# Performance work log

Hardware: AMD Instinct MI355X
Metric: run time of the kernel (lower is better)

The kernel has to match this reference:

```python
import jax, jax.numpy as jnp
import numpy as np


def setup_inputs() -> dict:
    key = jax.random.key(0)
    k1, k2, k3 = jax.random.split(key, 3)
    B, F, D = 8192, 4096, 1024
    x = jax.random.normal(k1, (B, D), dtype=jnp.float32)
    mu = jax.random.normal(k2, (F, D), dtype=jnp.float32)
    # keep scales strictly positive and well-conditioned
    scale_diag = jax.random.uniform(k3, (F, D), dtype=jnp.float32, minval=0.5, maxval=1.5)
    return {"x": x, "mu": mu, "scale_diag": scale_diag}


def reference(x, mu, scale_diag):
    # Unnormalized diag-Gaussian log prob for every (batch, feature) pair:
    #   out[b, f] = sum_d -0.5 * ((x[b,d] - mu[f,d]) / scale[f,d])^2
    # Expanded to GEMM form (quadratic expansion):
    #   -0.5 * ( x^2 @ inv2.T  -  2 * x @ (mu*inv2).T  +  sum_d mu^2*inv2 )
    inv2 = 1.0 / (scale_diag * scale_diag)            # [F, D]
    xx = jnp.matmul(x * x, inv2.T)                    # [B, F]
    xm = jnp.matmul(x, (mu * inv2).T)                 # [B, F]
    mm = jnp.sum(mu * mu * inv2, axis=-1)             # [F]
    return -0.5 * (xx - 2.0 * xm + mm[None, :])       # [B, F]
```

## Files before the change

### kernel.cpp

```cpp
#include <hip/hip_runtime.h>
#include <hip/hip_bf16.h>
#include <cstdint>

#define B_SZ 8192
#define F_SZ 4096
#define D_SZ 1024
#define K_SZ 2048

typedef __bf16 bf16x8 __attribute__((ext_vector_type(8)));
typedef float f32x4 __attribute__((ext_vector_type(4)));

__device__ __forceinline__ unsigned short f2bf(float f) {
    union { float f; unsigned u; } c; c.f = f;
    unsigned r = c.u + 0x7fff + ((c.u >> 16) & 1);
    return (unsigned short)(r >> 16);
}

__device__ __forceinline__ void async16(const void* g, void* l) {
    __builtin_amdgcn_global_load_lds(
        (__attribute__((address_space(1))) void*)g,
        (__attribute__((address_space(3))) void*)l, 16, 0, 0);
}

__global__ __launch_bounds__(256) void prep_a(const float* __restrict__ x,
                                              unsigned short* __restrict__ A) {
    int gid = blockIdx.x * 256 + threadIdx.x;
    int idx4 = gid * 4;
    int b = idx4 >> 10;
    int d = idx4 & 1023;
    float4 v = *(const float4*)(x + idx4);
    ushort4 xx, xs;
    xx.x = f2bf(v.x * v.x); xx.y = f2bf(v.y * v.y);
    xx.z = f2bf(v.z * v.z); xx.w = f2bf(v.w * v.w);
    xs.x = f2bf(v.x); xs.y = f2bf(v.y); xs.z = f2bf(v.z); xs.w = f2bf(v.w);
    size_t base = (size_t)b * K_SZ;
    *(ushort4*)(A + base + d) = xx;
    *(ushort4*)(A + base + 1024 + d) = xs;
}

__global__ __launch_bounds__(256) void prep_w(const float* __restrict__ mu,
                                              const float* __restrict__ sd,
                                              unsigned short* __restrict__ W,
                                              float* __restrict__ nmm) {
    int f = blockIdx.x;
    int d = threadIdx.x * 4;
    size_t off = (size_t)f * D_SZ + d;
    float4 m = *(const float4*)(mu + off);
    float4 s = *(const float4*)(sd + off);
    float i0 = 1.0f / (s.x * s.x), i1 = 1.0f / (s.y * s.y);
    float i2 = 1.0f / (s.z * s.z), i3 = 1.0f / (s.w * s.w);
    ushort4 wi, wm;
    wi.x = f2bf(i0); wi.y = f2bf(i1); wi.z = f2bf(i2); wi.w = f2bf(i3);
    wm.x = f2bf(-2.0f * m.x * i0); wm.y = f2bf(-2.0f * m.y * i1);
    wm.z = f2bf(-2.0f * m.z * i2); wm.w = f2bf(-2.0f * m.w * i3);
    size_t wb = (size_t)f * K_SZ + d;
    *(ushort4*)(W + wb) = wi;
    *(ushort4*)(W + wb + 1024) = wm;
    float mm = m.x * m.x * i0 + m.y * m.y * i1 + m.z * m.z * i2 + m.w * m.w * i3;
    #pragma unroll
    for (int o = 32; o > 0; o >>= 1) mm += __shfl_down(mm, o, 64);
    __shared__ float red[4];
    if ((threadIdx.x & 63) == 0) red[threadIdx.x >> 6] = mm;
    __syncthreads();
    if (threadIdx.x == 0) nmm[f] = -0.5f * (red[0] + red[1] + red[2] + red[3]);
}

__global__ __launch_bounds__(256) void gemm_bt(const unsigned short* __restrict__ A,
                                               const unsigned short* __restrict__ W,
                                               const float* __restrict__ nmm,
                                               float* __restrict__ out) {
    __shared__ __align__(16) unsigned short sA[128 * 32];
    __shared__ __align__(16) unsigned short sB[128 * 32];

    const int tid  = threadIdx.x;
    const int wave = tid >> 6;
    const int lane = tid & 63;
    const int wm = (wave >> 1) * 64;
    const int wn = (wave & 1) * 64;
    const int tileM = blockIdx.y * 128;
    const int tileN = blockIdx.x * 128;
    const int r16  = lane & 15;
    const int quad = lane >> 4;

    const int row0 = tid >> 2;
    const int col0 = (tid & 3) * 8;
    unsigned short* ldsA0 = sA + (wave * 64) * 8;
    unsigned short* ldsA1 = sA + (256 + wave * 64) * 8;
    unsigned short* ldsB0 = sB + (wave * 64) * 8;
    unsigned short* ldsB1 = sB + (256 + wave * 64) * 8;

    const f32x4 vzero = {0.f, 0.f, 0.f, 0.f};
    f32x4 acc[4][4];
    #pragma unroll
    for (int i = 0; i < 4; ++i)
        #pragma unroll
        for (int j = 0; j < 4; ++j) acc[i][j] = vzero;

    for (int k0 = 0; k0 < K_SZ; k0 += 32) {
        async16(A + (size_t)(tileM + row0) * K_SZ + k0 + col0, ldsA0);
        async16(A + (size_t)(tileM + row0 + 64) * K_SZ + k0 + col0, ldsA1);
        async16(W + (size_t)(tileN + row0) * K_SZ + k0 + col0, ldsB0);
        async16(W + (size_t)(tileN + row0 + 64) * K_SZ + k0 + col0, ldsB1);
        __syncthreads();

        bf16x8 af[4], bfr[4];
        #pragma unroll
        for (int i = 0; i < 4; ++i)
            af[i] = *(const bf16x8*)(sA + (wm + i * 16 + r16) * 32 + quad * 8);
        #pragma unroll
        for (int j = 0; j < 4; ++j)
            bfr[j] = *(const bf16x8*)(sB + (wn + j * 16 + r16) * 32 + quad * 8);
        #pragma unroll
        for (int i = 0; i < 4; ++i)
            #pragma unroll
            for (int j = 0; j < 4; ++j)
                acc[i][j] = __builtin_amdgcn_mfma_f32_16x16x32_bf16(
                    af[i], bfr[j], acc[i][j], 0, 0, 0);
        __syncthreads();
    }

    int   fc[4];
    float cj[4];
    #pragma unroll
    for (int j = 0; j < 4; ++j) {
        fc[j] = tileN + wn + j * 16 + r16;
        cj[j] = nmm[fc[j]];
    }
    #pragma unroll
    for (int i = 0; i < 4; ++i) {
        int mbase = tileM + wm + i * 16 + quad * 4;
        #pragma unroll
        for (int r = 0; r < 4; ++r) {
            float* orow = out + (size_t)(mbase + r) * F_SZ;
            #pragma unroll
            for (int j = 0; j < 4; ++j)
                orow[fc[j]] = -0.5f * acc[i][j][r] + cj[j];
        }
    }
}

extern "C" void kernel_launch(void* const* d_in, const int* in_sizes, int n_in,
                              void* d_out, int out_size, void* d_ws, size_t ws_size,
                              hipStream_t stream) {
    const float* x  = (const float*)d_in[0];
    const float* mu = (const float*)d_in[1];
    const float* sd = (const float*)d_in[2];
    float* out = (float*)d_out;

    unsigned short* A = (unsigned short*)d_ws;
    unsigned short* W = A + (size_t)B_SZ * K_SZ;
    float* nmm = (float*)(W + (size_t)F_SZ * K_SZ);

    prep_a<<<(B_SZ * D_SZ) / (256 * 4), 256, 0, stream>>>(x, A);
    prep_w<<<F_SZ, 256, 0, stream>>>(mu, sd, W, nmm);
    gemm_bt<<<dim3(F_SZ / 128, B_SZ / 128), 256, 0, stream>>>(A, W, nmm, out);
}
```

Before: 328.5 us.

## Merge prep kernels, remap GEMM tiles per XCD, use nontemporal loads/stores

Combines the two preprocessing kernels into one launch, so one launch and its gap go away. The GEMM block index is remapped so that each XCD (blocks with the same bid&7) works on a contiguous band of M rows across all N tiles, aiming for better L2 reuse of A tiles within an XCD. The fp32 inputs are read and the output is written with nontemporal hints so they do not pollute the cache. The mapping assumes 8 XCDs with round-robin block dispatch, and nontemporal stores could interact oddly with the write path.

```diff
diff --git a/kernel.cpp b/kernel.cpp
--- a/kernel.cpp
+++ b/kernel.cpp
@@ -9,6 +9,8 @@
 
 typedef __bf16 bf16x8 __attribute__((ext_vector_type(8)));
 typedef float f32x4 __attribute__((ext_vector_type(4)));
+typedef float fvec4 __attribute__((ext_vector_type(4)));
+typedef unsigned short u16x4 __attribute__((ext_vector_type(4)));
 
 __device__ __forceinline__ unsigned short f2bf(float f) {
     union { float f; unsigned u; } c; c.f = f;
@@ -22,47 +24,47 @@
         (__attribute__((address_space(3))) void*)l, 16, 0, 0);
 }
 
-__global__ __launch_bounds__(256) void prep_a(const float* __restrict__ x,
-                                              unsigned short* __restrict__ A) {
-    int gid = blockIdx.x * 256 + threadIdx.x;
-    int idx4 = gid * 4;
-    int b = idx4 >> 10;
-    int d = idx4 & 1023;
-    float4 v = *(const float4*)(x + idx4);
-    ushort4 xx, xs;
-    xx.x = f2bf(v.x * v.x); xx.y = f2bf(v.y * v.y);
-    xx.z = f2bf(v.z * v.z); xx.w = f2bf(v.w * v.w);
-    xs.x = f2bf(v.x); xs.y = f2bf(v.y); xs.z = f2bf(v.z); xs.w = f2bf(v.w);
-    size_t base = (size_t)b * K_SZ;
-    *(ushort4*)(A + base + d) = xx;
-    *(ushort4*)(A + base + 1024 + d) = xs;
-}
-
-__global__ __launch_bounds__(256) void prep_w(const float* __restrict__ mu,
-                                              const float* __restrict__ sd,
-                                              unsigned short* __restrict__ W,
-                                              float* __restrict__ nmm) {
-    int f = blockIdx.x;
-    int d = threadIdx.x * 4;
-    size_t off = (size_t)f * D_SZ + d;
-    float4 m = *(const float4*)(mu + off);
-    float4 s = *(const float4*)(sd + off);
-    float i0 = 1.0f / (s.x * s.x), i1 = 1.0f / (s.y * s.y);
-    float i2 = 1.0f / (s.z * s.z), i3 = 1.0f / (s.w * s.w);
-    ushort4 wi, wm;
-    wi.x = f2bf(i0); wi.y = f2bf(i1); wi.z = f2bf(i2); wi.w = f2bf(i3);
-    wm.x = f2bf(-2.0f * m.x * i0); wm.y = f2bf(-2.0f * m.y * i1);
-    wm.z = f2bf(-2.0f * m.z * i2); wm.w = f2bf(-2.0f * m.w * i3);
-    size_t wb = (size_t)f * K_SZ + d;
-    *(ushort4*)(W + wb) = wi;
-    *(ushort4*)(W + wb + 1024) = wm;
-    float mm = m.x * m.x * i0 + m.y * m.y * i1 + m.z * m.z * i2 + m.w * m.w * i3;
-    #pragma unroll
-    for (int o = 32; o > 0; o >>= 1) mm += __shfl_down(mm, o, 64);
-    __shared__ float red[4];
-    if ((threadIdx.x & 63) == 0) red[threadIdx.x >> 6] = mm;
-    __syncthreads();
-    if (threadIdx.x == 0) nmm[f] = -0.5f * (red[0] + red[1] + red[2] + red[3]);
+__global__ __launch_bounds__(256) void prep(const float* __restrict__ x,
+                                            const float* __restrict__ mu,
+                                            const float* __restrict__ sd,
+                                            unsigned short* __restrict__ A,
+                                            unsigned short* __restrict__ W,
+                                            float* __restrict__ nmm) {
+    const int tid = threadIdx.x;
+    const int d = tid * 4;
+    if (blockIdx.x < B_SZ) {
+        const int b = blockIdx.x;
+        fvec4 v = __builtin_nontemporal_load(
+            (const fvec4*)(x + (size_t)b * D_SZ + d));
+        u16x4 xx, xs;
+        xx.x = f2bf(v.x * v.x); xx.y = f2bf(v.y * v.y);
+        xx.z = f2bf(v.z * v.z); xx.w = f2bf(v.w * v.w);
+        xs.x = f2bf(v.x); xs.y = f2bf(v.y); xs.z = f2bf(v.z); xs.w = f2bf(v.w);
+        size_t base = (size_t)b * K_SZ;
+        *(u16x4*)(A + base + d) = xx;
+        *(u16x4*)(A + base + 1024 + d) = xs;
+    } else {
+        const int f = blockIdx.x - B_SZ;
+        size_t off = (size_t)f * D_SZ + d;
+        fvec4 m = __builtin_nontemporal_load((const fvec4*)(mu + off));
+        fvec4 s = __builtin_nontemporal_load((const fvec4*)(sd + off));
+        float i0 = 1.0f / (s.x * s.x), i1 = 1.0f / (s.y * s.y);
+        float i2 = 1.0f / (s.z * s.z), i3 = 1.0f / (s.w * s.w);
+        u16x4 wi, wm;
+        wi.x = f2bf(i0); wi.y = f2bf(i1); wi.z = f2bf(i2); wi.w = f2bf(i3);
+        wm.x = f2bf(-2.0f * m.x * i0); wm.y = f2bf(-2.0f * m.y * i1);
+        wm.z = f2bf(-2.0f * m.z * i2); wm.w = f2bf(-2.0f * m.w * i3);
+        size_t wb = (size_t)f * K_SZ + d;
+        *(u16x4*)(W + wb) = wi;
+        *(u16x4*)(W + wb + 1024) = wm;
+        float mm = m.x * m.x * i0 + m.y * m.y * i1 + m.z * m.z * i2 + m.w * m.w * i3;
+        #pragma unroll
+        for (int o = 32; o > 0; o >>= 1) mm += __shfl_down(mm, o, 64);
+        __shared__ float red[4];
+        if ((tid & 63) == 0) red[tid >> 6] = mm;
+        __syncthreads();
+        if (tid == 0) nmm[f] = -0.5f * (red[0] + red[1] + red[2] + red[3]);
+    }
 }
 
 __global__ __launch_bounds__(256) void gemm_bt(const unsigned short* __restrict__ A,
@@ -77,8 +79,13 @@
     const int lane = tid & 63;
     const int wm = (wave >> 1) * 64;
     const int wn = (wave & 1) * 64;
-    const int tileM = blockIdx.y * 128;
-    const int tileN = blockIdx.x * 128;
+
+    const int bid = blockIdx.x;
+    const int xcd = bid & 7;
+    const int g   = bid >> 3;
+    const int tileN = (g & 31) * 128;
+    const int tileM = (xcd * 8 + (g >> 5)) * 128;
+
     const int r16  = lane & 15;
     const int quad = lane >> 4;
 
@@ -134,7 +141,8 @@
             float* orow = out + (size_t)(mbase + r) * F_SZ;
             #pragma unroll
             for (int j = 0; j < 4; ++j)
-                orow[fc[j]] = -0.5f * acc[i][j][r] + cj[j];
+                __builtin_nontemporal_store(-0.5f * acc[i][j][r] + cj[j],
+                                            orow + fc[j]);
         }
     }
 }
@@ -151,7 +159,6 @@
     unsigned short* W = A + (size_t)B_SZ * K_SZ;
     float* nmm = (float*)(W + (size_t)F_SZ * K_SZ);
 
-    prep_a<<<(B_SZ * D_SZ) / (256 * 4), 256, 0, stream>>>(x, A);
-    prep_w<<<F_SZ, 256, 0, stream>>>(mu, sd, W, nmm);
-    gemm_bt<<<dim3(F_SZ / 128, B_SZ / 128), 256, 0, stream>>>(A, W, nmm, out);
+    prep<<<B_SZ + F_SZ, 256, 0, stream>>>(x, mu, sd, A, W, nmm);
+    gemm_bt<<<(B_SZ / 128) * (F_SZ / 128), 256, 0, stream>>>(A, W, nmm, out);
 }
```

Result: no change. 331.7 us (+1.0%).
